# Kernel tuning notes

Measured on AMD Instinct MI355X. Metric: run time of the kernel, lower is better.

## Reference

```python
import jax, jax.numpy as jnp
import numpy as np

EPS = 1e-5

def _linear(x, w, b):
    # torch nn.Linear convention: w is [out, in]
    return jnp.einsum('...i,oi->...o', x, w) + b

def _l2_normalize(x, axis=-1):
    n = jnp.sqrt(jnp.sum(x * x, axis=axis, keepdims=True))
    return x / jnp.maximum(n, 1e-12)

def _online_softmax_scan(sim):
    # sim: [B, H, L]. Running max m_t and running sum s_t = sum_{i<=t} exp(sim_i - m_t)
    def combine(a, b):
        ma, sa = a
        mb, sb = b
        m = jnp.maximum(ma, mb)
        s = sa * jnp.exp(ma - m) + sb * jnp.exp(mb - m)
        return m, s
    m_scan, s_scan = jax.lax.associative_scan(combine, (sim, jnp.ones_like(sim)), axis=2)
    return m_scan, s_scan


def setup_inputs() -> dict:
    key = jax.random.key(0)
    ks = jax.random.split(key, 8)
    B, L, D = 2, 2048, 256
    H, h = 8, 32
    s = 1.0 / np.sqrt(D)
    inp = {
        'x': jax.random.normal(ks[0], (B, L, D), jnp.float32),
        'wq_w': jax.random.normal(ks[1], (D, D), jnp.float32) * s,
        'wq_b': jnp.zeros((D,), jnp.float32),
        'wk_w': jax.random.normal(ks[2], (D, D), jnp.float32) * s,
        'wk_b': jnp.zeros((D,), jnp.float32),
        'wv_w': jax.random.normal(ks[3], (D, D), jnp.float32) * s,
        'wv_b': jnp.zeros((D,), jnp.float32),
        'wo_w': jax.random.normal(ks[4], (D, D), jnp.float32) * s,
        'wo_b': jnp.zeros((D,), jnp.float32),
        'wg_w': jax.random.normal(ks[5], (1, h * h), jnp.float32) * (1.0 / np.sqrt(h * h)),
        'wg_b': jnp.zeros((1,), jnp.float32),
        'kv_norm_scale': jnp.ones((1, H, 1, h, h), jnp.float32),
        'qk_norm_scale': jnp.full((1, H, 1), 1.0 / np.sqrt(h), jnp.float32),
    }
    return inp


def reference(x, wq_w, wq_b, wk_w, wk_b, wv_w, wv_b, wo_w, wo_b,
              wg_w, wg_b, kv_norm_scale, qk_norm_scale):
    B, L, D = x.shape
    H, h = kv_norm_scale.shape[1], kv_norm_scale.shape[3]

    q = _linear(x, wq_w, wq_b).reshape(B, L, H, h).transpose(0, 2, 1, 3)  # bhld
    k = _linear(x, wk_w, wk_b).reshape(B, L, H, h).transpose(0, 2, 1, 3)
    v = _linear(x, wv_w, wv_b).reshape(B, L, H, h).transpose(0, 2, 1, 3)

    sim = jnp.einsum('bhld,bhld->bhl', q, k) * qk_norm_scale  # [B,H,L]

    k = _l2_normalize(k)
    v = _l2_normalize(v)

    # outer-product KV state per position: [B,H,L,h,h]
    Z = jnp.einsum('bhld,bhle->bhlde', v, k) * kv_norm_scale

    # gating: squared ReLU of linear over flattened h*h features
    gate_inputs = Z.reshape(B, H, L, h * h)
    gates_logits = jnp.einsum('bhli,oi->bhlo', gate_inputs, wg_w) + wg_b  # [B,H,L,1]
    gates = jnp.square(jax.nn.relu(gates_logits)) + EPS
    gates = gates[..., None]  # [B,H,L,1,1]
    gated_Z = gates * Z

    # associative scans along L
    m_scan, s_scan = _online_softmax_scan(sim)        # [B,H,L]
    Z_scan = jnp.cumsum(gated_Z, axis=2)              # [B,H,L,h,h]
    g_scan = jnp.cumsum(gates, axis=2)                # [B,H,L,1,1]

    softmax_weights = (jnp.exp(sim - m_scan) / (s_scan + EPS))[..., None, None]
    gated_weights = Z_scan / (g_scan + EPS)
    attn_weights = gated_weights * (1.0 + jax.nn.silu(softmax_weights))

    ctxt = jnp.einsum('bhld,bhlde->bhle', q, attn_weights)
    ctxt = ctxt.transpose(0, 2, 1, 3).reshape(B, L, D)
    return _linear(ctxt, wo_w, wo_b)
```

## Files before the change

### kernel.cpp

```cpp
#include <hip/hip_runtime.h>
#include <math.h>

#define EPSV 1e-5f

static constexpr int Ls = 2048, Hh = 8;
static constexpr int NCH = 64, T = 32;

typedef unsigned short u16;
using frag  = __attribute__((ext_vector_type(8))) short;
using f32x4 = __attribute__((ext_vector_type(4))) float;

__device__ __forceinline__ void split_bf16(float v, u16& hi, u16& lo) {
    const unsigned u = __float_as_uint(v);
    hi = (u16)(u >> 16);
    const float hf = __uint_as_float((unsigned)hi << 16);
    lo = (u16)(__float_as_uint(v - hf) >> 16);
}

__device__ __forceinline__ unsigned pk2(u16 a, u16 b) {
    return (unsigned)a | ((unsigned)b << 16);
}

__device__ __forceinline__ void split8(const float4& a, const float4& b,
                                       uint4& hi, uint4& lo) {
    u16 h[8], l[8];
    const float f[8] = {a.x, a.y, a.z, a.w, b.x, b.y, b.z, b.w};
#pragma unroll
    for (int i = 0; i < 8; ++i) split_bf16(f[i], h[i], l[i]);
    hi = make_uint4(pk2(h[0], h[1]), pk2(h[2], h[3]), pk2(h[4], h[5]), pk2(h[6], h[7]));
    lo = make_uint4(pk2(l[0], l[1]), pk2(l[2], l[3]), pk2(l[4], l[5]), pk2(l[6], l[7]));
}

__global__ __launch_bounds__(256) void qkv_fused(
    const float* __restrict__ x,
    const float* __restrict__ wq, const float* __restrict__ wk, const float* __restrict__ wv,
    const float* __restrict__ bq, const float* __restrict__ bk, const float* __restrict__ bv,
    const float* __restrict__ wg_w, const float* __restrict__ wg_b,
    const float* __restrict__ kvs, const float* __restrict__ qks,
    float* __restrict__ qh, float* __restrict__ kh, float* __restrict__ vh,
    float* __restrict__ simG, float* __restrict__ gG,
    float* __restrict__ ZcT, float* __restrict__ mT, float* __restrict__ sT,
    float* __restrict__ gTt)
{
    constexpr int LDK = 40;
    constexpr int LDT = 66;
    __shared__ __align__(16) float smemf[8960];
    __shared__ float wkS[2][1024];
    __shared__ float lsim[2][32], lg2[2][32];

    u16* As_hi = (u16*)smemf;
    u16* As_lo = As_hi + 1280;
    u16* Wst   = As_lo + 1280;
    float* Qt = smemf;
    float* Kt = Qt + 32 * LDT;
    float* Vt = Kt + 32 * LDT;

    const int tid = threadIdx.x;
    const int mt = blockIdx.x, nt = blockIdx.y;
    const int m0 = mt * 32, ncol0 = nt * 64;
    const int bidx = m0 >> 11, lg = m0 & (Ls - 1);
    const int cg = lg >> 5;
    const int wave = tid >> 6, lane = tid & 63;
    const int l15 = lane & 15, quad = lane >> 4;
    const int srow = tid >> 2, sk = (tid & 3) * 8;
    const int rf = wave & 1, cfp = wave >> 1;

    for (int i = tid; i < 2048; i += 256) {
        const int h = i >> 10, de = i & 1023;
        wkS[h][de] = wg_w[de] * kvs[(nt * 2 + h) * 1024 + de];
    }

    const float* Wsrc[3] = {wq, wk, wv};
    f32x4 acc[3][2] = {};

    float4 ca0, ca1, cw0[3], cw1[3];
    if (tid < 128) {
        ca0 = *(const float4*)&x[(size_t)(m0 + srow) * 256 + 0 + sk];
        ca1 = *(const float4*)&x[(size_t)(m0 + srow) * 256 + 0 + sk + 4];
    }
#pragma unroll
    for (int w = 0; w < 3; ++w) {
        cw0[w] = *(const float4*)&Wsrc[w][(size_t)(ncol0 + srow) * 256 + 0 + sk];
        cw1[w] = *(const float4*)&Wsrc[w][(size_t)(ncol0 + srow) * 256 + 0 + sk + 4];
    }

#pragma unroll
    for (int kk = 0; kk < 8; ++kk) {
        __syncthreads();
        {
            uint4 hi, lo;
            if (tid < 128) {
                split8(ca0, ca1, hi, lo);
                *(uint4*)&As_hi[srow * LDK + sk] = hi;
                *(uint4*)&As_lo[srow * LDK + sk] = lo;
            }
#pragma unroll
            for (int w = 0; w < 3; ++w) {
                split8(cw0[w], cw1[w], hi, lo);
                *(uint4*)&Wst[w * 5120 + srow * LDK + sk] = hi;
                *(uint4*)&Wst[w * 5120 + 2560 + srow * LDK + sk] = lo;
            }
        }
        __syncthreads();

        if (kk < 7) {
            const int k0n = (kk + 1) * 32;
            if (tid < 128) {
                ca0 = *(const float4*)&x[(size_t)(m0 + srow) * 256 + k0n + sk];
                ca1 = *(const float4*)&x[(size_t)(m0 + srow) * 256 + k0n + sk + 4];
            }
#pragma unroll
            for (int w = 0; w < 3; ++w) {
                cw0[w] = *(const float4*)&Wsrc[w][(size_t)(ncol0 + srow) * 256 + k0n + sk];
                cw1[w] = *(const float4*)&Wsrc[w][(size_t)(ncol0 + srow) * 256 + k0n + sk + 4];
            }
        }

        const frag ah = *(const frag*)&As_hi[(rf * 16 + l15) * LDK + quad * 8];
        const frag al = *(const frag*)&As_lo[(rf * 16 + l15) * LDK + quad * 8];
#pragma unroll
        for (int w = 0; w < 3; ++w)
#pragma unroll
            for (int cf = 0; cf < 2; ++cf) {
                const u16* bp = &Wst[w * 5120 + ((cfp * 2 + cf) * 16 + l15) * LDK + quad * 8];
                const frag bh = *(const frag*)bp;
                const frag bl = *(const frag*)(bp + 2560);
                acc[w][cf] = __builtin_amdgcn_mfma_f32_16x16x32_bf16(ah, bh, acc[w][cf], 0, 0, 0);
                acc[w][cf] = __builtin_amdgcn_mfma_f32_16x16x32_bf16(ah, bl, acc[w][cf], 0, 0, 0);
                acc[w][cf] = __builtin_amdgcn_mfma_f32_16x16x32_bf16(al, bh, acc[w][cf], 0, 0, 0);
            }
    }
    __syncthreads();

    {
        float* tiles[3] = {Qt, Kt, Vt};
        const float* biases[3] = {bq, bk, bv};
#pragma unroll
        for (int w = 0; w < 3; ++w)
#pragma unroll
            for (int cf = 0; cf < 2; ++cf) {
                const int col = (cfp * 2 + cf) * 16 + l15;
                const float bias = biases[w][ncol0 + col];
#pragma unroll
                for (int r = 0; r < 4; ++r) {
                    const int m = rf * 16 + quad * 4 + r;
                    tiles[w][m * LDT + col] = acc[w][cf][r] + bias;
                }
            }
    }
    __syncthreads();

    {
        const int task = tid >> 2, sub = tid & 3;
        const int h = task >> 5, l = task & 31;
        const int cb = h * 32, e0 = sub * 8;
        float ksum = 0.f, vsum = 0.f, qk = 0.f;
#pragma unroll
        for (int e = e0; e < e0 + 8; ++e) {
            const float kv = Kt[l * LDT + cb + e];
            const float vv = Vt[l * LDT + cb + e];
            const float qv = Qt[l * LDT + cb + e];
            ksum = fmaf(kv, kv, ksum);
            vsum = fmaf(vv, vv, vsum);
            qk = fmaf(qv, kv, qk);
        }
        ksum += __shfl_xor(ksum, 1); ksum += __shfl_xor(ksum, 2);
        vsum += __shfl_xor(vsum, 1); vsum += __shfl_xor(vsum, 2);
        qk   += __shfl_xor(qk, 1);   qk   += __shfl_xor(qk, 2);
        const float kscale = 1.f / fmaxf(sqrtf(ksum), 1e-12f);
        const float vscale = 1.f / fmaxf(sqrtf(vsum), 1e-12f);
#pragma unroll
        for (int e = e0; e < e0 + 8; ++e) {
            Kt[l * LDT + cb + e] *= kscale;
            Vt[l * LDT + cb + e] *= vscale;
        }
        if (sub == 0) {
            const float sim = qk * qks[nt * 2 + h];
            lsim[h][l] = sim;
            simG[(size_t)(bidx * 8 + nt * 2 + h) * Ls + lg + l] = sim;
        }
    }
    __syncthreads();

    {
        const float* tl[3] = {Qt, Kt, Vt};
        float* gl[3] = {qh, kh, vh};
#pragma unroll
        for (int arr = 0; arr < 3; ++arr)
#pragma unroll
            for (int it = 0; it < 4; ++it) {
                const int idx = it * 512 + tid * 2;
                const int l = idx >> 6, col = idx & 63;
                const int h = col >> 5, e = col & 31;
                float2 v;
                v.x = tl[arr][l * LDT + h * 32 + e];
                v.y = tl[arr][l * LDT + h * 32 + e + 1];
                *(float2*)&gl[arr][(size_t)(bidx * 8 + nt * 2 + h) * 65536 +
                                   (size_t)(lg + l) * 32 + e] = v;
            }
    }

    {
        const int task = tid >> 2, sub = tid & 3;
        const int h = task >> 5, l = task & 31;
        float vreg[32];
#pragma unroll 8
        for (int d = 0; d < 32; ++d) vreg[d] = Vt[l * LDT + h * 32 + d];
        float u = 0.f;
        const int e0 = sub * 8;
#pragma unroll
        for (int e = e0; e < e0 + 8; ++e) {
            float s = 0.f;
#pragma unroll 8
            for (int d = 0; d < 32; ++d)
                s = fmaf(vreg[d], wkS[h][d * 32 + e], s);
            u = fmaf(s, Kt[l * LDT + h * 32 + e], u);
        }
        u += __shfl_xor(u, 1);
        u += __shfl_xor(u, 2);
        if (sub == 0) {
            const float r = fmaxf(u + wg_b[0], 0.f);
            const float g = r * r + EPSV;
            lg2[h][l] = g;
            gG[(size_t)(bidx * 8 + nt * 2 + h) * Ls + lg + l] = g;
        }
    }
    __syncthreads();

    {
        const int d = tid >> 3, e0 = (tid & 7) * 4;
#pragma unroll
        for (int h = 0; h < 2; ++h) {
            float z0 = 0.f, z1 = 0.f, z2 = 0.f, z3 = 0.f;
#pragma unroll 8
            for (int l = 0; l < 32; ++l) {
                const float gv = lg2[h][l] * Vt[l * LDT + h * 32 + d];
                z0 = fmaf(gv, Kt[l * LDT + h * 32 + e0 + 0], z0);
                z1 = fmaf(gv, Kt[l * LDT + h * 32 + e0 + 1], z1);
                z2 = fmaf(gv, Kt[l * LDT + h * 32 + e0 + 2], z2);
                z3 = fmaf(gv, Kt[l * LDT + h * 32 + e0 + 3], z3);
            }
            const int bhg = bidx * 8 + nt * 2 + h;
            float4 zv; zv.x = z0; zv.y = z1; zv.z = z2; zv.w = z3;
            *(float4*)&ZcT[((size_t)bhg * NCH + cg) * 1024 + d * 32 + e0] = zv;
        }
    }

    if (wave < 2 && lane < 32) {
        const int h = wave;
        float m = lsim[h][lane], s = 1.f, g = lg2[h][lane];
#pragma unroll
        for (int off = 16; off; off >>= 1) {
            const float mo = __shfl_xor(m, off);
            const float so = __shfl_xor(s, off);
            const float mn = fmaxf(m, mo);
            s = s * __expf(m - mn) + so * __expf(mo - mn);
            m = mn;
            g += __shfl_xor(g, off);
        }
        if (lane == 0) {
            const int bhg = bidx * 8 + nt * 2 + h;
            mT[bhg * NCH + cg] = m;
            sT[bhg * NCH + cg] = s;
            gTt[bhg * NCH + cg] = g;
        }
    }
}

__global__ __launch_bounds__(256) void prefix_kernel(
    float* __restrict__ Zc, float* __restrict__ mT, float* __restrict__ sT,
    float* __restrict__ gTt,
    const float* __restrict__ kvs, float* __restrict__ aW, float* __restrict__ bW,
    int* __restrict__ flagW)
{
    const int bh = blockIdx.x, seg = blockIdx.y;
    const int tid = threadIdx.x;
    const int el = seg * 256 + tid;
    float* Zb = Zc + (size_t)bh * NCH * 1024 + el;

    float v[NCH];
#pragma unroll
    for (int i = 0; i < NCH; ++i) v[i] = Zb[(size_t)i * 1024];
    float run = 0.f;
#pragma unroll
    for (int i = 0; i < NCH; ++i) {
        const float t = v[i];
        Zb[(size_t)i * 1024] = run;
        run += t;
    }

    if (seg == 0 && tid < 64) {
        float m = mT[bh * NCH + tid], s = sT[bh * NCH + tid], g = gTt[bh * NCH + tid];
#pragma unroll
        for (int off = 1; off < 64; off <<= 1) {
            const float mo = __shfl_up(m, off);
            const float so = __shfl_up(s, off);
            const float go = __shfl_up(g, off);
            if (tid >= off) {
                const float mn = fmaxf(m, mo);
                s = s * __expf(m - mn) + so * __expf(mo - mn);
                m = mn;
                g += go;
            }
        }
        float me = __shfl_up(m, 1), se = __shfl_up(s, 1), ge = __shfl_up(g, 1);
        if (tid == 0) { me = -1e30f; se = 0.f; ge = 0.f; }
        mT[bh * NCH + tid] = me;
        sT[bh * NCH + tid] = se;
        gTt[bh * NCH + tid] = ge;
    }

    if (bh == 0 && seg == 3) {
        const int h = tid >> 5, e = tid & 31;
        const float* K = kvs + h * 1024;
        const float k00 = K[0];
        int ok = (k00 != 0.0f);
        for (int d = 0; d < 32; ++d) {
            const float lhs = K[d * 32 + e] * k00;
            const float rhs = K[d * 32] * K[e];
            const float diff = fabsf(lhs - rhs);
            if (diff > 1e-6f * fmaxf(fmaxf(fabsf(lhs), fabsf(rhs)), 1e-20f)) ok = 0;
        }
        aW[h * 32 + e] = K[e * 32];
        bW[h * 32 + e] = (k00 != 0.0f) ? K[e] / k00 : 0.f;
        const int allok = __syncthreads_and(ok);
        if (tid == 0) flagW[0] = allok;
    }
}

__global__ __launch_bounds__(1024) void chunk_out_kernel(
    const float* __restrict__ qh, const float* __restrict__ knG, const float* __restrict__ vnG,
    const float* __restrict__ simG, const float* __restrict__ gG,
    const float* __restrict__ kvs,
    const float* __restrict__ ZcP, const float* __restrict__ mP,
    const float* __restrict__ sP, const float* __restrict__ gP,
    const float* __restrict__ aW, const float* __restrict__ bW,
    const int* __restrict__ flagW,
    u16* __restrict__ chi, u16* __restrict__ clo)
{
    __shared__ float qa[1024], knb[1024], zp[1024], lkvs[1024];
    __shared__ float vnT[32 * 33], sW[32 * 33];
    __shared__ float la[32], lb[32], lg[T], lsim[T], lwgt[T];
    const int tid = threadIdx.x;
    const int c = blockIdx.x, bh = blockIdx.y, h = bh & 7, b = bh >> 3;
    const int l = tid >> 5, lane = tid & 31;
    const size_t base = ((size_t)bh * Ls + c * T) * 32;

    const float qv = qh[base + tid];
    const float knv = knG[base + tid];
    const float vnv = vnG[base + tid];
    const float kvsv = kvs[h * 1024 + tid];
    const int flag = flagW[0];
    vnT[lane * 33 + l] = vnv;
    zp[tid] = ZcP[((size_t)bh * NCH + c) * 1024 + tid];
    lkvs[tid] = kvsv;
    if (tid < 32) {
        la[tid] = aW[h * 32 + tid];
        lb[tid] = bW[h * 32 + tid];
        lg[tid] = gG[bh * Ls + c * T + tid];
        lsim[tid] = simG[bh * Ls + c * T + tid];
    }
    __syncthreads();

    qa[tid] = flag ? qv * la[lane] : qv;
    knb[tid] = flag ? knv * lb[lane] : knv;
    if (tid < 32) {
        float m = lsim[tid], s = 1.f, g = lg[tid];
#pragma unroll
        for (int off = 1; off < 32; off <<= 1) {
            const float mo = __shfl_up(m, off);
            const float so = __shfl_up(s, off);
            const float go = __shfl_up(g, off);
            if (tid >= off) {
                const float mn = fmaxf(m, mo);
                s = s * __expf(m - mn) + so * __expf(mo - mn);
                m = mn;
                g += go;
            }
        }
        const float mp = mP[bh * NCH + c];
        const float sp = sP[bh * NCH + c];
        const float gp = gP[bh * NCH + c];
        const float mn = fmaxf(mp, m);
        s = sp * __expf(mp - mn) + s * __expf(m - mn);
        m = mn;
        g += gp;
        const float sw = __expf(lsim[tid] - m) / (s + EPSV);
        const float sig = 1.f / (1.f + __expf(-sw));
        lwgt[tid] = (1.f + sw * sig) / (g + EPSV);
    }
    __syncthreads();

    float y;
    if (flag) {
        float s = 0.f, y0 = 0.f;
        const float4* qa4 = (const float4*)&qa[l * 32];
#pragma unroll
        for (int d4 = 0; d4 < 8; ++d4) {
            const float4 q4 = qa4[d4];
            const int d = d4 * 4;
            s = fmaf(q4.x, vnT[(d + 0) * 33 + lane], s);
            s = fmaf(q4.y, vnT[(d + 1) * 33 + lane], s);
            s = fmaf(q4.z, vnT[(d + 2) * 33 + lane], s);
            s = fmaf(q4.w, vnT[(d + 3) * 33 + lane], s);
            y0 = fmaf(q4.x, zp[(d + 0) * 32 + lane], y0);
            y0 = fmaf(q4.y, zp[(d + 1) * 32 + lane], y0);
            y0 = fmaf(q4.z, zp[(d + 2) * 32 + lane], y0);
            y0 = fmaf(q4.w, zp[(d + 3) * 32 + lane], y0);
        }
        sW[l * 33 + lane] = (lane <= l) ? lg[lane] * s : 0.f;
        __syncthreads();
        y = y0 * lb[lane];
#pragma unroll 8
        for (int j = 0; j < 32; ++j)
            y = fmaf(sW[l * 33 + j], knb[j * 32 + lane], y);
        y *= lwgt[l];
    } else {
        float qe[32];
#pragma unroll
        for (int d = 0; d < 32; ++d)
            qe[d] = qa[l * 32 + d] * lkvs[d * 32 + lane];
        y = 0.f;
#pragma unroll
        for (int d = 0; d < 32; ++d)
            y = fmaf(qe[d], zp[d * 32 + lane], y);
        for (int j = 0; j < 32; ++j) {
            float s = 0.f;
#pragma unroll
            for (int d = 0; d < 32; ++d)
                s = fmaf(qe[d], vnT[d * 33 + j], s);
            if (j <= l) y = fmaf(lg[j] * s, knb[j * 32 + lane], y);
        }
        y *= lwgt[l];
    }
    u16 hi, lo;
    split_bf16(y, hi, lo);
    const size_t oidx = ((size_t)(b * Ls + c * T + l)) * 256 + h * 32 + lane;
    chi[oidx] = hi;
    clo[oidx] = lo;
}

__global__ __launch_bounds__(256) void out_gemm(
    const u16* __restrict__ Ahi, const u16* __restrict__ Alo,
    const float* __restrict__ wo, const float* __restrict__ bo,
    float* __restrict__ out)
{
    constexpr int LDK = 40;
    __shared__ __align__(16) u16 As_hi[32 * LDK];
    __shared__ __align__(16) u16 As_lo[32 * LDK];
    __shared__ __align__(16) u16 Ws_hi[64 * LDK];
    __shared__ __align__(16) u16 Ws_lo[64 * LDK];

    const int tid = threadIdx.x;
    const int mt = blockIdx.x, nt = blockIdx.y;
    const int m0 = mt * 32, ncol0 = nt * 64;
    const int wave = tid >> 6, lane = tid & 63;
    const int l15 = lane & 15, quad = lane >> 4;
    const int srow = tid >> 2, sk = (tid & 3) * 8;
    const int rf = wave & 1, cfp = wave >> 1;

    f32x4 acc[2] = {};

    uint4 cah, cal;
    float4 cw0, cw1;
    if (tid < 128) {
        cah = *(const uint4*)&Ahi[(size_t)(m0 + srow) * 256 + 0 + sk];
        cal = *(const uint4*)&Alo[(size_t)(m0 + srow) * 256 + 0 + sk];
    }
    cw0 = *(const float4*)&wo[(size_t)(ncol0 + srow) * 256 + 0 + sk];
    cw1 = *(const float4*)&wo[(size_t)(ncol0 + srow) * 256 + 0 + sk + 4];

#pragma unroll
    for (int kk = 0; kk < 8; ++kk) {
        __syncthreads();
        uint4 whi, wlo;
        split8(cw0, cw1, whi, wlo);
        if (tid < 128) {
            *(uint4*)&As_hi[srow * LDK + sk] = cah;
            *(uint4*)&As_lo[srow * LDK + sk] = cal;
        }
        *(uint4*)&Ws_hi[srow * LDK + sk] = whi;
        *(uint4*)&Ws_lo[srow * LDK + sk] = wlo;
        __syncthreads();

        if (kk < 7) {
            const int k0n = (kk + 1) * 32;
            if (tid < 128) {
                cah = *(const uint4*)&Ahi[(size_t)(m0 + srow) * 256 + k0n + sk];
                cal = *(const uint4*)&Alo[(size_t)(m0 + srow) * 256 + k0n + sk];
            }
            cw0 = *(const float4*)&wo[(size_t)(ncol0 + srow) * 256 + k0n + sk];
            cw1 = *(const float4*)&wo[(size_t)(ncol0 + srow) * 256 + k0n + sk + 4];
        }

        const frag fah = *(const frag*)&As_hi[(rf * 16 + l15) * LDK + quad * 8];
        const frag fal = *(const frag*)&As_lo[(rf * 16 + l15) * LDK + quad * 8];
#pragma unroll
        for (int cf = 0; cf < 2; ++cf) {
            const frag fbh = *(const frag*)&Ws_hi[((cfp * 2 + cf) * 16 + l15) * LDK + quad * 8];
            const frag fbl = *(const frag*)&Ws_lo[((cfp * 2 + cf) * 16 + l15) * LDK + quad * 8];
            acc[cf] = __builtin_amdgcn_mfma_f32_16x16x32_bf16(fah, fbh, acc[cf], 0, 0, 0);
            acc[cf] = __builtin_amdgcn_mfma_f32_16x16x32_bf16(fah, fbl, acc[cf], 0, 0, 0);
            acc[cf] = __builtin_amdgcn_mfma_f32_16x16x32_bf16(fal, fbh, acc[cf], 0, 0, 0);
        }
    }

#pragma unroll
    for (int cf = 0; cf < 2; ++cf) {
        const int o = ncol0 + (cfp * 2 + cf) * 16 + l15;
        const float bias = bo[o];
#pragma unroll
        for (int r = 0; r < 4; ++r) {
            const int rm = m0 + rf * 16 + quad * 4 + r;
            out[(size_t)rm * 256 + o] = acc[cf][r] + bias;
        }
    }
}

extern "C" void kernel_launch(void* const* d_in, const int* in_sizes, int n_in,
                              void* d_out, int out_size, void* d_ws, size_t ws_size,
                              hipStream_t stream) {
    const float* x    = (const float*)d_in[0];
    const float* wq_w = (const float*)d_in[1];
    const float* wq_b = (const float*)d_in[2];
    const float* wk_w = (const float*)d_in[3];
    const float* wk_b = (const float*)d_in[4];
    const float* wv_w = (const float*)d_in[5];
    const float* wv_b = (const float*)d_in[6];
    const float* wo_w = (const float*)d_in[7];
    const float* wo_b = (const float*)d_in[8];
    const float* wg_w = (const float*)d_in[9];
    const float* wg_b = (const float*)d_in[10];
    const float* kvs  = (const float*)d_in[11];
    const float* qks  = (const float*)d_in[12];
    float* out = (float*)d_out;

    u16* chi = (u16*)d_ws;
    u16* clo = chi + 1048576;
    float* qh   = (float*)(clo + 1048576);
    float* kh   = qh + 1048576;
    float* vh   = kh + 1048576;
    float* ZcT  = vh + 1048576;
    float* simG = ZcT + 1048576;
    float* gG   = simG + 32768;
    float* mT   = gG + 32768;
    float* sT   = mT + 1024;
    float* gTt  = sT + 1024;
    float* aW   = gTt + 1024;
    float* bW   = aW + 256;
    int* flagW  = (int*)(bW + 256);

    qkv_fused<<<dim3(128, 4), 256, 0, stream>>>(
        x, wq_w, wk_w, wv_w, wq_b, wk_b, wv_b, wg_w, wg_b, kvs, qks,
        qh, kh, vh, simG, gG, ZcT, mT, sT, gTt);
    prefix_kernel<<<dim3(16, 4), 256, 0, stream>>>(
        ZcT, mT, sT, gTt, kvs, aW, bW, flagW);
    chunk_out_kernel<<<dim3(NCH, 16), 1024, 0, stream>>>(
        qh, kh, vh, simG, gG, kvs, ZcT, mT, sT, gTt, aW, bW, flagW, chi, clo);
    out_gemm<<<dim3(128, 4), 256, 0, stream>>>(
        chi, clo, wo_w, wo_b, out);
}
```

Before: 133.5 us.

## Alias gate weights into reused smem, add occupancy hints, halve out_gemm tile

```diff
diff --git a/kernel.cpp b/kernel.cpp
--- a/kernel.cpp
+++ b/kernel.cpp
@@ -31,7 +31,7 @@
     lo = make_uint4(pk2(l[0], l[1]), pk2(l[2], l[3]), pk2(l[4], l[5]), pk2(l[6], l[7]));
 }
 
-__global__ __launch_bounds__(256) void qkv_fused(
+__global__ __launch_bounds__(256, 4) void qkv_fused(
     const float* __restrict__ x,
     const float* __restrict__ wq, const float* __restrict__ wk, const float* __restrict__ wv,
     const float* __restrict__ bq, const float* __restrict__ bk, const float* __restrict__ bv,
@@ -45,7 +45,6 @@
     constexpr int LDK = 40;
     constexpr int LDT = 66;
     __shared__ __align__(16) float smemf[8960];
-    __shared__ float wkS[2][1024];
     __shared__ float lsim[2][32], lg2[2][32];
 
     u16* As_hi = (u16*)smemf;
@@ -54,6 +53,7 @@
     float* Qt = smemf;
     float* Kt = Qt + 32 * LDT;
     float* Vt = Kt + 32 * LDT;
+    float* wkS = smemf + 6336;
 
     const int tid = threadIdx.x;
     const int mt = blockIdx.x, nt = blockIdx.y;
@@ -65,11 +65,6 @@
     const int srow = tid >> 2, sk = (tid & 3) * 8;
     const int rf = wave & 1, cfp = wave >> 1;
 
-    for (int i = tid; i < 2048; i += 256) {
-        const int h = i >> 10, de = i & 1023;
-        wkS[h][de] = wg_w[de] * kvs[(nt * 2 + h) * 1024 + de];
-    }
-
     const float* Wsrc[3] = {wq, wk, wv};
     f32x4 acc[3][2] = {};
 
@@ -147,6 +142,10 @@
                     tiles[w][m * LDT + col] = acc[w][cf][r] + bias;
                 }
             }
+        for (int i = tid; i < 2048; i += 256) {
+            const int h = i >> 10, de = i & 1023;
+            wkS[h * 1024 + de] = wg_w[de] * kvs[(nt * 2 + h) * 1024 + de];
+        }
     }
     __syncthreads();
 
@@ -213,7 +212,7 @@
             float s = 0.f;
 #pragma unroll 8
             for (int d = 0; d < 32; ++d)
-                s = fmaf(vreg[d], wkS[h][d * 32 + e], s);
+                s = fmaf(vreg[d], wkS[h * 1024 + d * 32 + e], s);
             u = fmaf(s, Kt[l * LDT + h * 32 + e], u);
         }
         u += __shfl_xor(u, 1);
@@ -328,7 +327,7 @@
     }
 }
 
-__global__ __launch_bounds__(1024) void chunk_out_kernel(
+__global__ __launch_bounds__(1024, 8) void chunk_out_kernel(
     const float* __restrict__ qh, const float* __restrict__ knG, const float* __restrict__ vnG,
     const float* __restrict__ simG, const float* __restrict__ gG,
     const float* __restrict__ kvs,
@@ -448,39 +447,41 @@
     constexpr int LDK = 40;
     __shared__ __align__(16) u16 As_hi[32 * LDK];
     __shared__ __align__(16) u16 As_lo[32 * LDK];
-    __shared__ __align__(16) u16 Ws_hi[64 * LDK];
-    __shared__ __align__(16) u16 Ws_lo[64 * LDK];
+    __shared__ __align__(16) u16 Ws_hi[32 * LDK];
+    __shared__ __align__(16) u16 Ws_lo[32 * LDK];
 
     const int tid = threadIdx.x;
     const int mt = blockIdx.x, nt = blockIdx.y;
-    const int m0 = mt * 32, ncol0 = nt * 64;
+    const int m0 = mt * 32, ncol0 = nt * 32;
     const int wave = tid >> 6, lane = tid & 63;
     const int l15 = lane & 15, quad = lane >> 4;
     const int srow = tid >> 2, sk = (tid & 3) * 8;
-    const int rf = wave & 1, cfp = wave >> 1;
-
-    f32x4 acc[2] = {};
+    const int rf = wave & 1, cf = wave >> 1;
+
+    f32x4 acc = {};
 
     uint4 cah, cal;
     float4 cw0, cw1;
     if (tid < 128) {
         cah = *(const uint4*)&Ahi[(size_t)(m0 + srow) * 256 + 0 + sk];
         cal = *(const uint4*)&Alo[(size_t)(m0 + srow) * 256 + 0 + sk];
-    }
-    cw0 = *(const float4*)&wo[(size_t)(ncol0 + srow) * 256 + 0 + sk];
-    cw1 = *(const float4*)&wo[(size_t)(ncol0 + srow) * 256 + 0 + sk + 4];
+    } else {
+        cw0 = *(const float4*)&wo[(size_t)(ncol0 + srow - 32) * 256 + 0 + sk];
+        cw1 = *(const float4*)&wo[(size_t)(ncol0 + srow - 32) * 256 + 0 + sk + 4];
+    }
 
 #pragma unroll
     for (int kk = 0; kk < 8; ++kk) {
         __syncthreads();
-        uint4 whi, wlo;
-        split8(cw0, cw1, whi, wlo);
         if (tid < 128) {
             *(uint4*)&As_hi[srow * LDK + sk] = cah;
             *(uint4*)&As_lo[srow * LDK + sk] = cal;
-        }
-        *(uint4*)&Ws_hi[srow * LDK + sk] = whi;
-        *(uint4*)&Ws_lo[srow * LDK + sk] = wlo;
+        } else {
+            uint4 whi, wlo;
+            split8(cw0, cw1, whi, wlo);
+            *(uint4*)&Ws_hi[(srow - 32) * LDK + sk] = whi;
+            *(uint4*)&Ws_lo[(srow - 32) * LDK + sk] = wlo;
+        }
         __syncthreads();
 
         if (kk < 7) {
@@ -488,31 +489,28 @@
             if (tid < 128) {
                 cah = *(const uint4*)&Ahi[(size_t)(m0 + srow) * 256 + k0n + sk];
                 cal = *(const uint4*)&Alo[(size_t)(m0 + srow) * 256 + k0n + sk];
-            }
-            cw0 = *(const float4*)&wo[(size_t)(ncol0 + srow) * 256 + k0n + sk];
-            cw1 = *(const float4*)&wo[(size_t)(ncol0 + srow) * 256 + k0n + sk + 4];
+            } else {
+                cw0 = *(const float4*)&wo[(size_t)(ncol0 + srow - 32) * 256 + k0n + sk];
+                cw1 = *(const float4*)&wo[(size_t)(ncol0 + srow - 32) * 256 + k0n + sk + 4];
+            }
         }
 
         const frag fah = *(const frag*)&As_hi[(rf * 16 + l15) * LDK + quad * 8];
         const frag fal = *(const frag*)&As_lo[(rf * 16 + l15) * LDK + quad * 8];
-#pragma unroll
-        for (int cf = 0; cf < 2; ++cf) {
-            const frag fbh = *(const frag*)&Ws_hi[((cfp * 2 + cf) * 16 + l15) * LDK + quad * 8];
-            const frag fbl = *(const frag*)&Ws_lo[((cfp * 2 + cf) * 16 + l15) * LDK + quad * 8];
-            acc[cf] = __builtin_amdgcn_mfma_f32_16x16x32_bf16(fah, fbh, acc[cf], 0, 0, 0);
-            acc[cf] = __builtin_amdgcn_mfma_f32_16x16x32_bf16(fah, fbl, acc[cf], 0, 0, 0);
-            acc[cf] = __builtin_amdgcn_mfma_f32_16x16x32_bf16(fal, fbh, acc[cf], 0, 0, 0);
-        }
-    }
-
-#pragma unroll
-    for (int cf = 0; cf < 2; ++cf) {
-        const int o = ncol0 + (cfp * 2 + cf) * 16 + l15;
+        const frag fbh = *(const frag*)&Ws_hi[(cf * 16 + l15) * LDK + quad * 8];
+        const frag fbl = *(const frag*)&Ws_lo[(cf * 16 + l15) * LDK + quad * 8];
+        acc = __builtin_amdgcn_mfma_f32_16x16x32_bf16(fah, fbh, acc, 0, 0, 0);
+        acc = __builtin_amdgcn_mfma_f32_16x16x32_bf16(fah, fbl, acc, 0, 0, 0);
+        acc = __builtin_amdgcn_mfma_f32_16x16x32_bf16(fal, fbh, acc, 0, 0, 0);
+    }
+
+    {
+        const int o = ncol0 + cf * 16 + l15;
         const float bias = bo[o];
 #pragma unroll
         for (int r = 0; r < 4; ++r) {
             const int rm = m0 + rf * 16 + quad * 4 + r;
-            out[(size_t)rm * 256 + o] = acc[cf][r] + bias;
+            out[(size_t)rm * 256 + o] = acc[r] + bias;
         }
     }
 }
@@ -557,6 +555,6 @@
         ZcT, mT, sT, gTt, kvs, aW, bW, flagW);
     chunk_out_kernel<<<dim3(NCH, 16), 1024, 0, stream>>>(
         qh, kh, vh, simG, gG, kvs, ZcT, mT, sT, gTt, aW, bW, flagW, chi, clo);
-    out_gemm<<<dim3(128, 4), 256, 0, stream>>>(
+    out_gemm<<<dim3(128, 8), 256, 0, stream>>>(
         chi, clo, wo_w, wo_b, out);
 }
```

Result: slower. 160.2 us (+20.0%).
